# Performance work log

Hardware: AMD Instinct MI355X
Metric: run time of the kernel (lower is better)

The kernel has to match this reference:

```python
import jax, jax.numpy as jnp
import numpy as np

B, I, J, WIDTH, NH = 8, 1024, 1024, 512, 8
HD = WIDTH // NH
SCALE = WIDTH ** (-0.5)  # NOTE: original scales by width**-0.5, not head_dim**-0.5


def setup_inputs() -> dict:
    key = jax.random.key(0)
    ks = jax.random.split(key, 7)
    return {
        "q": jax.random.normal(ks[0], (B, I, WIDTH), dtype=jnp.float32),
        "k": jax.random.normal(ks[1], (B, J, WIDTH), dtype=jnp.float32),
        "v": jax.random.normal(ks[2], (B, J, WIDTH), dtype=jnp.float32),
        "Wq": jax.random.normal(ks[3], (WIDTH, WIDTH), dtype=jnp.float32) * (WIDTH ** -0.5),
        "Wk": jax.random.normal(ks[4], (WIDTH, WIDTH), dtype=jnp.float32) * (WIDTH ** -0.5),
        "Wv": jax.random.normal(ks[5], (WIDTH, WIDTH), dtype=jnp.float32) * (WIDTH ** -0.5),
        "Wo": jax.random.normal(ks[6], (WIDTH, WIDTH), dtype=jnp.float32) * (WIDTH ** -0.5),
    }


def reference(q, k, v, Wq, Wk, Wv, Wo):
    b, i, _ = q.shape
    j = k.shape[1]
    # Linear(bias=False): y = x @ W.T
    qh = (q @ Wq.T).reshape(b, NH, i, HD)  # faithful to torch .view(b, n, i, d) (no transpose)
    kh = (k @ Wk.T).reshape(b, NH, j, HD)
    vh = (v @ Wv.T).reshape(b, NH, j, HD)
    attn_score = jnp.einsum('bnid,bnjd->bnij', qh, kh) * SCALE
    attn_weight = jax.nn.softmax(attn_score, axis=3)
    # drop_prob = 0.0 -> dropout is identity
    x = jnp.einsum('bnij,bnjd->bnid', attn_weight, vh)
    x = x.transpose(0, 2, 1, 3).reshape(b, i, NH * HD)  # b n i d -> b i (n d)
    x = x @ Wo.T
    return (x, attn_weight)
```

## Files before the change

### kernel.cpp

```cpp
#include <hip/hip_runtime.h>
#include <hip/hip_bf16.h>


typedef __hip_bfloat16 bf16;
typedef __attribute__((ext_vector_type(8))) short bf16x8;
typedef __attribute__((ext_vector_type(4))) float f32x4;

#define BATCH 8
#define SEQ   1024
#define WIDTH 512
#define NHEAD 8
#define HD    64
#define SCALE_F 0.044194173824159216f

static __device__ __forceinline__ unsigned short f2bf(float x) {
  union { float f; unsigned u; } a; a.f = x;
  unsigned r = a.u + 0x7fffu + ((a.u >> 16) & 1u);
  return (unsigned short)(r >> 16);
}
static __device__ __forceinline__ float bf2f(unsigned short u) {
  union { unsigned u; float f; } a; a.u = ((unsigned)u) << 16; return a.f;
}

static __device__ __forceinline__ void gload_lds16(const void* g, void* l) {
  __builtin_amdgcn_global_load_lds((const __attribute__((address_space(1))) void*)g,
                                   (__attribute__((address_space(3))) void*)l,
                                   16, 0, 0);
}

static __device__ __forceinline__ bf16x8 frag_ld(const short* tile, int row, int c16) {
  int p = c16 ^ (row & 7);
  return *(const bf16x8*)(tile + row*64 + p*8);
}

__global__ void cast_all_kernel(const float* __restrict__ q, const float* __restrict__ k,
                                const float* __restrict__ v, const float* __restrict__ wq,
                                const float* __restrict__ wk, const float* __restrict__ wv,
                                const float* __restrict__ wo, bf16* __restrict__ wsb) {
  const long NQ = 1048576;
  const long NW = 65536;
  long g = (long)blockIdx.x * blockDim.x + threadIdx.x;
  const float* src; bf16* dst; long o;
  if (g < 3*NQ) {
    int t = (int)(g / NQ); o = g - (long)t*NQ;
    src = (t==0) ? q : ((t==1) ? k : v);
    dst = wsb + (size_t)t * 4194304;
  } else {
    long g2 = g - 3*NQ;
    if (g2 >= 4*NW) return;
    int t = (int)(g2 / NW); o = g2 - (long)t*NW;
    src = (t==0) ? wq : ((t==1) ? wk : ((t==2) ? wv : wo));
    dst = wsb + (size_t)3*4194304 + (size_t)t * 262144;
  }
  float4 f = ((const float4*)src)[o];
  ushort4 r4;
  r4.x = f2bf(f.x); r4.y = f2bf(f.y); r4.z = f2bf(f.z); r4.w = f2bf(f.w);
  ((ushort4*)dst)[o] = r4;
}

template<int F32OUT, int NZ>
__global__ __launch_bounds__(256) void gemm_bt(const bf16* __restrict__ A0, const bf16* __restrict__ A1,
                                               const bf16* __restrict__ A2, const bf16* __restrict__ W0,
                                               const bf16* __restrict__ W1, const bf16* __restrict__ W2,
                                               void* __restrict__ C0, void* __restrict__ C1,
                                               void* __restrict__ C2) {
  __shared__ short As[2][128*64];
  __shared__ short Bs[2][128*64];

  const int bid = blockIdx.x;
  const int xcd = bid & 7;
  const int idx = bid >> 3;
  const int g   = xcd * (8*NZ) + (idx >> 2);
  const int y   = idx & 3;
  const int z   = g >> 6;
  const int m   = g & 63;

  const bf16* A; const bf16* Bw; void* Cout;
  if (NZ == 1 || z == 0) { A = A0; Bw = W0; Cout = C0; }
  else if (z == 1)       { A = A1; Bw = W1; Cout = C1; }
  else                   { A = A2; Bw = W2; Cout = C2; }

  const int lane = threadIdx.x & 63;
  const int wid  = threadIdx.x >> 6;
  const int m0 = m * 128;
  const int n0 = y * 128;
  const int wm = (wid >> 1) * 64;
  const int wn = (wid & 1) * 64;
  const int lrow = lane >> 3;
  const int swz  = ((lane & 7) ^ lrow) * 8;

  const f32x4 zero4 = {0.f,0.f,0.f,0.f};
  f32x4 acc[4][4];
  for (int i=0;i<4;++i) for (int j=0;j<4;++j) acc[i][j] = zero4;

  auto stage = [&](int buf, int t) {
    const int k0 = t * 64;
    for (int i = 0; i < 4; ++i) {
      int c = wid*4 + i;
      int row = c*8 + lrow;
      gload_lds16(A  + (size_t)(m0 + row)*WIDTH + k0 + swz, &As[buf][c*512]);
      gload_lds16(Bw + (size_t)(n0 + row)*WIDTH + k0 + swz, &Bs[buf][c*512]);
    }
  };

  stage(0, 0);
  asm volatile("s_waitcnt vmcnt(0)" ::: "memory");
  __syncthreads();
  int cur = 0;

  for (int t = 0; t < 8; ++t) {
    if (t < 7) stage(cur ^ 1, t + 1);
    for (int kc = 0; kc < 2; ++kc) {
      bf16x8 af[4], bfr[4];
      for (int mf=0; mf<4; ++mf) af[mf]  = frag_ld(&As[cur][0], wm + mf*16 + (lane&15), (lane>>4) + kc*4);
      for (int nf=0; nf<4; ++nf) bfr[nf] = frag_ld(&Bs[cur][0], wn + nf*16 + (lane&15), (lane>>4) + kc*4);
      for (int mf=0; mf<4; ++mf)
        for (int nf=0; nf<4; ++nf)
          acc[mf][nf] = __builtin_amdgcn_mfma_f32_16x16x32_bf16(af[mf], bfr[nf], acc[mf][nf], 0,0,0);
    }
    if (t < 7) {
      asm volatile("s_waitcnt vmcnt(0)" ::: "memory");
      __syncthreads();
      cur ^= 1;
    }
  }
  for (int mf=0; mf<4; ++mf)
    for (int nf=0; nf<4; ++nf) {
      int col = n0 + wn + nf*16 + (lane & 15);
      for (int r=0; r<4; ++r) {
        int row = m0 + wm + mf*16 + (lane>>4)*4 + r;
        if (F32OUT)
          ((float*)Cout)[(size_t)row*WIDTH + col] = acc[mf][nf][r];
        else
          ((unsigned short*)Cout)[(size_t)row*WIDTH + col] = f2bf(acc[mf][nf][r]);
      }
    }
}

__global__ __launch_bounds__(256) void transpose_v(const bf16* __restrict__ Vh,
                                                   bf16* __restrict__ Vt) {
  __shared__ short t[64][72];
  int h  = blockIdx.x >> 4;
  int j0 = (blockIdx.x & 15) * 64;
  const bf16* src = Vh + (size_t)h * (SEQ*HD);
  bf16* dst = Vt + (size_t)h * (SEQ*HD);
  int tid = threadIdx.x;
  int r  = tid >> 2;
  int c0 = (tid & 3) * 16;
  bf16x8 v0 = *(const bf16x8*)(src + (size_t)(j0 + r)*HD + c0);
  bf16x8 v1 = *(const bf16x8*)(src + (size_t)(j0 + r)*HD + c0 + 8);
  for (int i = 0; i < 8; ++i) { t[r][c0+i] = v0[i]; t[r][c0+8+i] = v1[i]; }
  __syncthreads();
  bf16x8 w0, w1;
  for (int i = 0; i < 8; ++i) { w0[i] = t[c0+i][r]; w1[i] = t[c0+8+i][r]; }
  *(bf16x8*)(dst + (size_t)r*SEQ + j0 + c0)     = w0;
  *(bf16x8*)(dst + (size_t)r*SEQ + j0 + c0 + 8) = w1;
}

__global__ __launch_bounds__(256) void attn_kernel(const bf16* __restrict__ Qh,
                                                   const bf16* __restrict__ Kh,
                                                   const bf16* __restrict__ Vt,
                                                   float* __restrict__ attn_out,
                                                   bf16* __restrict__ ctx) {
  __shared__ short Ks[2][64*64];
  __shared__ short Vs[2][64*64];
  __shared__ short Ws[4][16*64];

  const int lane = threadIdx.x & 63;
  const int wid  = threadIdx.x >> 6;
  const int bid  = blockIdx.x;
  const int xcd  = bid & 7;
  const int idx  = bid >> 3;
  const int h    = xcd*8 + (idx >> 4);
  const int i0   = (idx & 15) * 64;
  const int b  = h >> 3;
  const int nh = h & 7;

  const bf16* Qhead  = Qh + (size_t)h * (SEQ*HD);
  const bf16* Khead  = Kh + (size_t)h * (SEQ*HD);
  const bf16* Vthead = Vt + (size_t)h * (SEQ*HD);

  const int lrow = lane >> 3;
  const int swz  = ((lane & 7) ^ lrow) * 8;

  const int qrow = i0 + wid*16 + (lane & 15);
  bf16x8 qf[2];
  qf[0] = *(const bf16x8*)(Qhead + (size_t)qrow*HD + (lane>>4)*8);
  qf[1] = *(const bf16x8*)(Qhead + (size_t)qrow*HD + 32 + (lane>>4)*8);

  const f32x4 zero4 = {0.f,0.f,0.f,0.f};

  auto stageK = [&](int buf, int jt) {
    const int j0 = jt * 64;
    for (int i = 0; i < 2; ++i) {
      int c = wid*2 + i;
      gload_lds16(Khead + (size_t)(j0 + c*8 + lrow)*HD + swz, &Ks[buf][c*512]);
    }
  };
  auto stageV = [&](int buf, int jt) {
    const int j0 = jt * 64;
    for (int i = 0; i < 2; ++i) {
      int c = wid*2 + i;
      gload_lds16(Vthead + (size_t)(c*8 + lrow)*SEQ + j0 + swz, &Vs[buf][c*512]);
    }
  };

  float lsum[4] = {0.f,0.f,0.f,0.f};
  stageK(0, 0);
  asm volatile("s_waitcnt vmcnt(0)" ::: "memory");
  __syncthreads();
  int cur = 0;
  for (int jt = 0; jt < 16; ++jt) {
    if (jt < 15) stageK(cur ^ 1, jt + 1);
    f32x4 sac[4] = {zero4, zero4, zero4, zero4};
    __builtin_amdgcn_s_setprio(1);
    for (int kc = 0; kc < 2; ++kc)
      for (int jf = 0; jf < 4; ++jf) {
        bf16x8 kf = frag_ld(&Ks[cur][0], jf*16 + (lane & 15), (lane>>4) + kc*4);
        sac[jf] = __builtin_amdgcn_mfma_f32_16x16x32_bf16(qf[kc], kf, sac[jf], 0, 0, 0);
      }
    __builtin_amdgcn_s_setprio(0);
    for (int jf = 0; jf < 4; ++jf)
      for (int r = 0; r < 4; ++r)
        lsum[r] += __expf(sac[jf][r] * SCALE_F);
    if (jt < 15) {
      asm volatile("s_waitcnt vmcnt(0)" ::: "memory");
      __syncthreads();
      cur ^= 1;
    }
  }
  for (int m = 1; m < 16; m <<= 1)
    for (int r = 0; r < 4; ++r)
      lsum[r] += __shfl_xor(lsum[r], m, 64);
  float linv[4];
  for (int r = 0; r < 4; ++r) linv[r] = 1.0f / lsum[r];
  __syncthreads();

  f32x4 cacc[4] = {zero4, zero4, zero4, zero4};
  short* Wsw = &Ws[wid][0];
  float* awbase = attn_out + (size_t)((size_t)h*SEQ + i0 + wid*16)*SEQ;
  stageK(0, 0); stageV(0, 0);
  asm volatile("s_waitcnt vmcnt(0)" ::: "memory");
  __syncthreads();
  cur = 0;
  for (int jt = 0; jt < 16; ++jt) {
    if (jt < 15) { stageK(cur ^ 1, jt + 1); stageV(cur ^ 1, jt + 1); }
    const int j0 = jt * 64;
    f32x4 sac[4] = {zero4, zero4, zero4, zero4};
    __builtin_amdgcn_s_setprio(1);
    for (int kc = 0; kc < 2; ++kc)
      for (int jf = 0; jf < 4; ++jf) {
        bf16x8 kf = frag_ld(&Ks[cur][0], jf*16 + (lane & 15), (lane>>4) + kc*4);
        sac[jf] = __builtin_amdgcn_mfma_f32_16x16x32_bf16(qf[kc], kf, sac[jf], 0, 0, 0);
      }
    __builtin_amdgcn_s_setprio(0);
    for (int jf = 0; jf < 4; ++jf)
      for (int r = 0; r < 4; ++r) {
        float w = __expf(sac[jf][r] * SCALE_F) * linv[r];
        int row = (lane>>4)*4 + r;
        int col = jf*16 + (lane & 15);
        Wsw[row*64 + (((col>>3) ^ (row & 7))<<3) + (col & 7)] = (short)f2bf(w);
      }
    asm volatile("s_waitcnt lgkmcnt(0)" ::: "memory");
    __builtin_amdgcn_s_setprio(1);
    for (int kc = 0; kc < 2; ++kc) {
      bf16x8 wa = frag_ld(Wsw, lane & 15, (lane>>4) + kc*4);
      for (int df = 0; df < 4; ++df) {
        bf16x8 vb = frag_ld(&Vs[cur][0], df*16 + (lane & 15), (lane>>4) + kc*4);
        cacc[df] = __builtin_amdgcn_mfma_f32_16x16x32_bf16(wa, vb, cacc[df], 0, 0, 0);
      }
    }
    __builtin_amdgcn_s_setprio(0);
    #pragma unroll
    for (int s = 0; s < 4; ++s) {
      int row = (lane>>4) + s*4;
      int lu  = (lane & 15) >> 1;
      uint2 pv = *(const uint2*)(Wsw + row*64 + ((lu ^ (row & 7)) << 3) + (lane & 1)*4);
      float4 o;
      o.x = bf2f((unsigned short)(pv.x & 0xffff));
      o.y = bf2f((unsigned short)(pv.x >> 16));
      o.z = bf2f((unsigned short)(pv.y & 0xffff));
      o.w = bf2f((unsigned short)(pv.y >> 16));
      *(float4*)(awbase + (size_t)row*SEQ + j0 + (lane & 15)*4) = o;
    }
    if (jt < 15) {
      asm volatile("s_waitcnt vmcnt(16) lgkmcnt(0)" ::: "memory");
      __builtin_amdgcn_s_barrier();
      cur ^= 1;
    }
  }
  for (int df = 0; df < 4; ++df)
    for (int r = 0; r < 4; ++r) {
      int irow = i0 + wid*16 + (lane>>4)*4 + r;
      ((unsigned short*)ctx)[(size_t)(b*SEQ + irow)*WIDTH + nh*HD + df*16 + (lane & 15)]
          = f2bf(cacc[df][r]);
    }
}

extern "C" void kernel_launch(void* const* d_in, const int* in_sizes, int n_in,
                              void* d_out, int out_size, void* d_ws, size_t ws_size,
                              hipStream_t stream) {
  const float* q  = (const float*)d_in[0];
  const float* k  = (const float*)d_in[1];
  const float* v  = (const float*)d_in[2];
  const float* wq = (const float*)d_in[3];
  const float* wk = (const float*)d_in[4];
  const float* wv = (const float*)d_in[5];
  const float* wo = (const float*)d_in[6];

  bf16* wsb = (bf16*)d_ws;
  bf16* qb  = wsb;
  bf16* kb  = qb + 4194304;
  bf16* vb  = kb + 4194304;
  bf16* wqb = vb + 4194304;
  bf16* wkb = wqb + 262144;
  bf16* wvb = wkb + 262144;
  bf16* wob = wvb + 262144;
  bf16* Qh  = wob + 262144;
  bf16* Kh  = Qh + 4194304;
  bf16* Vh  = Kh + 4194304;
  bf16* Vt  = Vh + 4194304;
  bf16* ctx = Vt + 4194304;

  float* x_out    = (float*)d_out;
  float* attn_out = (float*)d_out + 4194304;

  cast_all_kernel<<<13312, 256, 0, stream>>>(q, k, v, wq, wk, wv, wo, wsb);
  gemm_bt<0,3><<<768, 256, 0, stream>>>(qb, kb, vb, wqb, wkb, wvb,
                                        (void*)Qh, (void*)Kh, (void*)Vh);
  transpose_v<<<1024, 256, 0, stream>>>(Vh, Vt);
  attn_kernel<<<1024, 256, 0, stream>>>(Qh, Kh, Vt, attn_out, ctx);
  gemm_bt<1,1><<<256, 256, 0, stream>>>(ctx, nullptr, nullptr, wob, nullptr, nullptr,
                                        (void*)x_out, nullptr, nullptr);
}
```

Baseline: 144.0 us.

## Drop V transpose kernel; gather V fragments directly from global memory

Result: slower. 159.9 us (+11.0%).

```diff
diff --git a/kernel.cpp b/kernel.cpp
--- a/kernel.cpp
+++ b/kernel.cpp
@@ -137,33 +137,12 @@
     }
 }
 
-__global__ __launch_bounds__(256) void transpose_v(const bf16* __restrict__ Vh,
-                                                   bf16* __restrict__ Vt) {
-  __shared__ short t[64][72];
-  int h  = blockIdx.x >> 4;
-  int j0 = (blockIdx.x & 15) * 64;
-  const bf16* src = Vh + (size_t)h * (SEQ*HD);
-  bf16* dst = Vt + (size_t)h * (SEQ*HD);
-  int tid = threadIdx.x;
-  int r  = tid >> 2;
-  int c0 = (tid & 3) * 16;
-  bf16x8 v0 = *(const bf16x8*)(src + (size_t)(j0 + r)*HD + c0);
-  bf16x8 v1 = *(const bf16x8*)(src + (size_t)(j0 + r)*HD + c0 + 8);
-  for (int i = 0; i < 8; ++i) { t[r][c0+i] = v0[i]; t[r][c0+8+i] = v1[i]; }
-  __syncthreads();
-  bf16x8 w0, w1;
-  for (int i = 0; i < 8; ++i) { w0[i] = t[c0+i][r]; w1[i] = t[c0+8+i][r]; }
-  *(bf16x8*)(dst + (size_t)r*SEQ + j0 + c0)     = w0;
-  *(bf16x8*)(dst + (size_t)r*SEQ + j0 + c0 + 8) = w1;
-}
-
 __global__ __launch_bounds__(256) void attn_kernel(const bf16* __restrict__ Qh,
                                                    const bf16* __restrict__ Kh,
-                                                   const bf16* __restrict__ Vt,
+                                                   const bf16* __restrict__ Vh,
                                                    float* __restrict__ attn_out,
                                                    bf16* __restrict__ ctx) {
   __shared__ short Ks[2][64*64];
-  __shared__ short Vs[2][64*64];
   __shared__ short Ws[4][16*64];
 
   const int lane = threadIdx.x & 63;
@@ -178,7 +157,7 @@
 
   const bf16* Qhead  = Qh + (size_t)h * (SEQ*HD);
   const bf16* Khead  = Kh + (size_t)h * (SEQ*HD);
-  const bf16* Vthead = Vt + (size_t)h * (SEQ*HD);
+  const short* Vhead = (const short*)(Vh + (size_t)h * (SEQ*HD));
 
   const int lrow = lane >> 3;
   const int swz  = ((lane & 7) ^ lrow) * 8;
@@ -195,13 +174,6 @@
     for (int i = 0; i < 2; ++i) {
       int c = wid*2 + i;
       gload_lds16(Khead + (size_t)(j0 + c*8 + lrow)*HD + swz, &Ks[buf][c*512]);
-    }
-  };
-  auto stageV = [&](int buf, int jt) {
-    const int j0 = jt * 64;
-    for (int i = 0; i < 2; ++i) {
-      int c = wid*2 + i;
-      gload_lds16(Vthead + (size_t)(c*8 + lrow)*SEQ + j0 + swz, &Vs[buf][c*512]);
     }
   };
 
@@ -239,12 +211,12 @@
   f32x4 cacc[4] = {zero4, zero4, zero4, zero4};
   short* Wsw = &Ws[wid][0];
   float* awbase = attn_out + (size_t)((size_t)h*SEQ + i0 + wid*16)*SEQ;
-  stageK(0, 0); stageV(0, 0);
+  stageK(0, 0);
   asm volatile("s_waitcnt vmcnt(0)" ::: "memory");
   __syncthreads();
   cur = 0;
   for (int jt = 0; jt < 16; ++jt) {
-    if (jt < 15) { stageK(cur ^ 1, jt + 1); stageV(cur ^ 1, jt + 1); }
+    if (jt < 15) stageK(cur ^ 1, jt + 1);
     const int j0 = jt * 64;
     f32x4 sac[4] = {zero4, zero4, zero4, zero4};
     __builtin_amdgcn_s_setprio(1);
@@ -265,10 +237,18 @@
     __builtin_amdgcn_s_setprio(1);
     for (int kc = 0; kc < 2; ++kc) {
       bf16x8 wa = frag_ld(Wsw, lane & 15, (lane>>4) + kc*4);
+      bf16x8 vb[4];
+      #pragma unroll
       for (int df = 0; df < 4; ++df) {
-        bf16x8 vb = frag_ld(&Vs[cur][0], df*16 + (lane & 15), (lane>>4) + kc*4);
-        cacc[df] = __builtin_amdgcn_mfma_f32_16x16x32_bf16(wa, vb, cacc[df], 0, 0, 0);
-      }
+        const int jb = j0 + kc*32 + (lane>>4)*8;
+        const int d  = df*16 + (lane & 15);
+        #pragma unroll
+        for (int e = 0; e < 8; ++e)
+          vb[df][e] = Vhead[(size_t)(jb + e)*64 + d];
+      }
+      #pragma unroll
+      for (int df = 0; df < 4; ++df)
+        cacc[df] = __builtin_amdgcn_mfma_f32_16x16x32_bf16(wa, vb[df], cacc[df], 0, 0, 0);
     }
     __builtin_amdgcn_s_setprio(0);
     #pragma unroll
@@ -319,8 +299,7 @@
   bf16* Qh  = wob + 262144;
   bf16* Kh  = Qh + 4194304;
   bf16* Vh  = Kh + 4194304;
-  bf16* Vt  = Vh + 4194304;
-  bf16* ctx = Vt + 4194304;
+  bf16* ctx = Vh + 4194304;
 
   float* x_out    = (float*)d_out;
   float* attn_out = (float*)d_out + 4194304;
@@ -328,8 +307,7 @@
   cast_all_kernel<<<13312, 256, 0, stream>>>(q, k, v, wq, wk, wv, wo, wsb);
   gemm_bt<0,3><<<768, 256, 0, stream>>>(qb, kb, vb, wqb, wkb, wvb,
                                         (void*)Qh, (void*)Kh, (void*)Vh);
-  transpose_v<<<1024, 256, 0, stream>>>(Vh, Vt);
-  attn_kernel<<<1024, 256, 0, stream>>>(Qh, Kh, Vt, attn_out, ctx);
+  attn_kernel<<<1024, 256, 0, stream>>>(Qh, Kh, Vh, attn_out, ctx);
   gemm_bt<1,1><<<256, 256, 0, stream>>>(ctx, nullptr, nullptr, wob, nullptr, nullptr,
                                         (void*)x_out, nullptr, nullptr);
 }
```
